# Performance work log

Hardware: AMD Instinct MI355X
Metric: run time of the kernel (lower is better)

## Reference

```python
import jax, jax.numpy as jnp
import numpy as np
import math

LOG2PI = math.log(2.0 * math.pi)
ALPHA, BETA, GAMMA = 1.0, 4.0, 1.0  # coefficients (mi, tc, dw_kl)


def gaussian_log_density(samples, mean, log_var):
    inv_sigma = jnp.exp(-log_var)
    tmp = samples - mean
    return -0.5 * (tmp * tmp * inv_sigma + log_var + LOG2PI)


def log_importance_weight_matrix(batch_size, dataset_size):
    # Faithful port of the TF/beta-tcvae MSS importance weights.
    N = float(dataset_size)
    M = batch_size - 1
    strat_weight = (N - M) / (N * M)
    W = jnp.full((batch_size, batch_size), 1.0 / M, dtype=jnp.float32)
    W = W.at[:, 0].set(1.0 / N)
    W = W.at[:, 1].set(strat_weight)
    W = W.at[M - 1, 0].set(strat_weight)
    return jnp.log(W)


def setup_inputs() -> dict:
    key = jax.random.key(0)
    k1, k2, k3, k4, k5 = jax.random.split(key, 5)
    B, D, F = 2048, 16, 512
    return {
        "x": jax.random.normal(k1, (B, F), dtype=jnp.float32),
        "reconstruction": jax.random.normal(k2, (B, F), dtype=jnp.float32),
        "mu": jax.random.normal(k3, (B, D), dtype=jnp.float32),
        "log_var": jax.random.normal(k4, (B, D), dtype=jnp.float32) * 0.5,
        "z": jax.random.normal(k5, (B, D), dtype=jnp.float32),
        "size_dataset": 100000,
    }


def reference(x, reconstruction, mu, log_var, z, size_dataset):
    B = z.shape[0]
    # reconstruction loss: mean over batch of per-sample MAE == global mean abs error
    recon_loss = jnp.mean(jnp.abs(x - reconstruction))

    # log q(z|x): [B]
    log_q_zx = jnp.sum(gaussian_log_density(z, mu, log_var), axis=-1)

    # pairwise densities: [B, B, D]  (z_i under q(.|x_j))
    log_qz_prob = gaussian_log_density(z[:, None, :], mu[None, :, :], log_var[None, :, :])

    # log p(z): note the original passes ones_like(z) as log_var (faithful quirk)
    log_prior = jnp.sum(
        gaussian_log_density(z, jnp.zeros_like(z), jnp.ones_like(z)), axis=-1
    )

    # MSS importance weights [B, B]
    logiw = log_importance_weight_matrix(B, size_dataset)

    # log q(z): logsumexp over batch of joint densities + weights
    log_qz = jax.nn.logsumexp(jnp.sum(log_qz_prob, axis=2) + logiw, axis=1)  # [B]

    # log prod_d q(z_d): dimension-wise logsumexp then sum over dims
    log_qz_product = jnp.sum(
        jax.nn.logsumexp(log_qz_prob + logiw[:, :, None], axis=1), axis=1
    )  # [B]

    mutual_info_loss = jnp.mean(log_q_zx - log_qz)
    tc_loss = jnp.mean(log_qz - log_qz_product)
    dimension_wise_kl = jnp.mean(log_qz_product - log_prior)

    total_loss = (
        recon_loss
        + ALPHA * mutual_info_loss
        + BETA * tc_loss
        + GAMMA * dimension_wise_kl
    )
    return total_loss
```

## Files before the change

kernel.cpp:

```cpp
#include <hip/hip_runtime.h>
#include <math.h>

#define LOG2PI_F 1.8378770664093453f
#define LOG2E_F  1.4426950408889634f
#define LN2_F    0.6931471805599453f
#define EXP_NEG1 0.36787944117144233f

#define TI   32
#define JSP  16
#define JCH  128
#define ROWF 52

__device__ __forceinline__ float exp2_(float x) { return __builtin_amdgcn_exp2f(x); }
__device__ __forceinline__ float log2_(float x) { return __builtin_amdgcn_logf(x); }


__global__ __launch_bounds__(256) void k_prep_recon(
        const float* __restrict__ mu, const float* __restrict__ lv,
        const float* __restrict__ z, const int* __restrict__ nds,
        const float4* __restrict__ x, const float4* __restrict__ r,
        float* __restrict__ AC, float* __restrict__ PPa, float* __restrict__ PPb,
        float* __restrict__ RP, int B, int n4, int prepBlks) {
    __shared__ float ra[4], rb[4];
    const int lane = threadIdx.x & 63, wv = threadIdx.x >> 6;

    if ((int)blockIdx.x < prepBlks) {
        int idx = blockIdx.x * 256 + threadIdx.x;
        int j = idx >> 4, d = idx & 15;
        float m = mu[idx], l = lv[idx], zz = z[idx];
        float is = __expf(-l);
        float a = -0.5f * LOG2E_F * is;
        float b = -2.0f * a * m;
        float ec = fmaf(-0.5f * LOG2E_F, l + LOG2PI_F, a * m * m);

        float Nf = (float)(*nds);
        float Mf = (float)(B - 1);
        float strat = (Nf - Mf) / (Nf * Mf);
        float w = (j == 0) ? (1.0f / Nf) : ((j == 1) ? strat : (1.0f / Mf));

        float* row = AC + (size_t)j * ROWF;
        row[d] = a;
        row[16 + d] = b;
        row[32 + d] = w * exp2_(ec);
        float es = ec;
        es += __shfl_xor(es, 1); es += __shfl_xor(es, 2);
        es += __shfl_xor(es, 4); es += __shfl_xor(es, 8);
        if (d == 0) row[48] = w * exp2_(es);

        float t = zz - m;
        float ga = -0.5f * (fmaf(t * t, is, l) + LOG2PI_F);
        float gb = -0.5f * (fmaf(zz * zz, EXP_NEG1, 1.0f) + LOG2PI_F);
        #pragma unroll
        for (int off = 32; off > 0; off >>= 1) { ga += __shfl_down(ga, off); gb += __shfl_down(gb, off); }
        if (lane == 0) { ra[wv] = ga; rb[wv] = gb; }
        __syncthreads();
        if (threadIdx.x == 0) {
            PPa[blockIdx.x] = ra[0] + ra[1] + ra[2] + ra[3];
            PPb[blockIdx.x] = rb[0] + rb[1] + rb[2] + rb[3];
        }
    } else {
        int bid = blockIdx.x - prepBlks;
        float s = 0.0f;
        for (int idx = bid * 256 + threadIdx.x; idx < n4; idx += 512 * 256) {
            float4 a = x[idx], b = r[idx];
            s += fabsf(a.x - b.x) + fabsf(a.y - b.y) + fabsf(a.z - b.z) + fabsf(a.w - b.w);
        }
        #pragma unroll
        for (int off = 32; off > 0; off >>= 1) s += __shfl_down(s, off);
        if (lane == 0) ra[wv] = s;
        __syncthreads();
        if (threadIdx.x == 0) RP[bid] = ra[0] + ra[1] + ra[2] + ra[3];
    }
}

#define DIM2(AQ, BQ, CQ, comp, dd, SA, SB) \
    e = fmaf(AQ.comp, va2[dd], BQ.comp * va[dd]); SA += e; sda[dd] = fmaf(CQ.comp, exp2_(e), sda[dd]); \
    e = fmaf(AQ.comp, vb2[dd], BQ.comp * vb[dd]); SB += e; sdb[dd] = fmaf(CQ.comp, exp2_(e), sdb[dd]);

__global__ __launch_bounds__(256) void k_pair(const float* __restrict__ AC,
                                              const float* __restrict__ z,
                                              float* __restrict__ Rs,
                                              int B, int jch) {
    __shared__ float sbuf[JCH * ROWF];
    __shared__ float red[4][TI][17];

    const int il = threadIdx.x & 15;
    const int jg = threadIdx.x >> 4;
    const int i0 = blockIdx.x * TI + il;
    const int jbase = blockIdx.y * jch;

    {
        const float4* g = (const float4*)(AC + (size_t)jbase * ROWF);
        float4* dst = (float4*)sbuf;
        #pragma unroll
        for (int k = 0; k < 7; ++k) {
            int idx = threadIdx.x + k * 256;
            if (idx < (JCH * ROWF) / 4) dst[idx] = g[idx];
        }
    }

    float va[16], va2[16], vb[16], vb2[16];
    {
        const float4* zp = (const float4*)(z + (size_t)i0 * 16);
        float4 z0 = zp[0], z1 = zp[1], z2 = zp[2], z3 = zp[3];
        va[0]=z0.x; va[1]=z0.y; va[2]=z0.z; va[3]=z0.w;
        va[4]=z1.x; va[5]=z1.y; va[6]=z1.z; va[7]=z1.w;
        va[8]=z2.x; va[9]=z2.y; va[10]=z2.z; va[11]=z2.w;
        va[12]=z3.x; va[13]=z3.y; va[14]=z3.z; va[15]=z3.w;
        const float4* zq = (const float4*)(z + (size_t)(i0 + 16) * 16);
        float4 y0 = zq[0], y1 = zq[1], y2 = zq[2], y3 = zq[3];
        vb[0]=y0.x; vb[1]=y0.y; vb[2]=y0.z; vb[3]=y0.w;
        vb[4]=y1.x; vb[5]=y1.y; vb[6]=y1.z; vb[7]=y1.w;
        vb[8]=y2.x; vb[9]=y2.y; vb[10]=y2.z; vb[11]=y2.w;
        vb[12]=y3.x; vb[13]=y3.y; vb[14]=y3.z; vb[15]=y3.w;
        #pragma unroll
        for (int d = 0; d < 16; d++) { va2[d] = va[d] * va[d]; vb2[d] = vb[d] * vb[d]; }
    }

    float sda[16], sdb[16];
    #pragma unroll
    for (int d = 0; d < 16; d++) { sda[d] = 0.0f; sdb[d] = 0.0f; }
    float stA = 0.0f, stB = 0.0f;

    __syncthreads();

    const int nk = jch >> 4;
    for (int k = 0; k < nk; ++k) {
        const float* rp = sbuf + (jg + 16 * k) * ROWF;
        const float4* r4 = (const float4*)rp;
        float sa0 = 0.0f, sa1 = 0.0f, sb0 = 0.0f, sb1 = 0.0f, e;
        {
            float4 A0 = r4[0], A1 = r4[1], Bq0 = r4[4], Bq1 = r4[5], C0 = r4[8], C1 = r4[9];
            DIM2(A0, Bq0, C0, x, 0, sa0, sb0)  DIM2(A0, Bq0, C0, y, 1, sa1, sb1)
            DIM2(A0, Bq0, C0, z, 2, sa0, sb0)  DIM2(A0, Bq0, C0, w, 3, sa1, sb1)
            DIM2(A1, Bq1, C1, x, 4, sa0, sb0)  DIM2(A1, Bq1, C1, y, 5, sa1, sb1)
            DIM2(A1, Bq1, C1, z, 6, sa0, sb0)  DIM2(A1, Bq1, C1, w, 7, sa1, sb1)
        }
        {
            float4 A2 = r4[2], A3 = r4[3], Bq2 = r4[6], Bq3 = r4[7], C2 = r4[10], C3 = r4[11];
            DIM2(A2, Bq2, C2, x, 8, sa0, sb0)  DIM2(A2, Bq2, C2, y, 9, sa1, sb1)
            DIM2(A2, Bq2, C2, z, 10, sa0, sb0) DIM2(A2, Bq2, C2, w, 11, sa1, sb1)
            DIM2(A3, Bq3, C3, x, 12, sa0, sb0) DIM2(A3, Bq3, C3, y, 13, sa1, sb1)
            DIM2(A3, Bq3, C3, z, 14, sa0, sb0) DIM2(A3, Bq3, C3, w, 15, sa1, sb1)
        }
        float P = rp[48];
        stA = fmaf(P, exp2_(sa0 + sa1), stA);
        stB = fmaf(P, exp2_(sb0 + sb1), stB);
    }

    #pragma unroll
    for (int msk = 16; msk <= 32; msk <<= 1) {
        stA += __shfl_xor(stA, msk);
        stB += __shfl_xor(stB, msk);
        #pragma unroll
        for (int d = 0; d < 16; d++) {
            sda[d] += __shfl_xor(sda[d], msk);
            sdb[d] += __shfl_xor(sdb[d], msk);
        }
    }
    const int lane = threadIdx.x & 63, wv = threadIdx.x >> 6;
    if (lane < 16) {
        red[wv][lane][0] = stA;
        red[wv][lane + 16][0] = stB;
        #pragma unroll
        for (int d = 0; d < 16; d++) {
            red[wv][lane][1 + d] = sda[d];
            red[wv][lane + 16][1 + d] = sdb[d];
        }
    }
    __syncthreads();
    for (int t = threadIdx.x; t < TI * 17; t += 256) {
        int il2 = t & 31, c = t >> 5;
        float s = red[0][il2][c] + red[1][il2][c] + red[2][il2][c] + red[3][il2][c];
        Rs[((size_t)blockIdx.y * 17 + c) * B + blockIdx.x * TI + il2] = s;
    }
}

__global__ __launch_bounds__(256) void k_logs(const float* __restrict__ Rs,
                                              const float* __restrict__ AC,
                                              const float* __restrict__ z,
                                              const int* __restrict__ nds,
                                              float* __restrict__ LPa,
                                              float* __restrict__ LPb, int B) {
    int i = blockIdx.x * 256 + threadIdx.x;
    float S = 0.0f, Sd[16];
    #pragma unroll
    for (int d = 0; d < 16; d++) Sd[d] = 0.0f;
    for (int sp = 0; sp < JSP; ++sp) {
        const float* base = Rs + (size_t)sp * 17 * B + i;
        S += base[0];
        #pragma unroll
        for (int d = 0; d < 16; d++) Sd[d] += base[(size_t)(1 + d) * B];
    }

    if (i == B - 2) {
        const float* row0 = AC;
        const float* vv = z + (size_t)i * 16;
        float Nf = (float)(*nds);
        float Mf = (float)(B - 1);
        float strat = (Nf - Mf) / (Nf * Mf);
        float dwN = (strat - 1.0f / Nf) * Nf;
        float s2 = 0.0f;
        #pragma unroll
        for (int d = 0; d < 16; d++) {
            float vd = vv[d];
            float e = fmaf(row0[d], vd * vd, row0[16 + d] * vd);
            s2 += e;
            Sd[d] += dwN * row0[32 + d] * exp2_(e);
        }
        S += dwN * row0[48] * exp2_(s2);
    }

    float lqz = log2_(S) * LN2_F;
    float lqzp = 0.0f;
    #pragma unroll
    for (int d = 0; d < 16; d++) lqzp += log2_(Sd[d]);
    lqzp *= LN2_F;

    #pragma unroll
    for (int off = 32; off > 0; off >>= 1) {
        lqz += __shfl_down(lqz, off);
        lqzp += __shfl_down(lqzp, off);
    }
    __shared__ float ra[4], rb[4];
    int lane = threadIdx.x & 63, wv = threadIdx.x >> 6;
    if (lane == 0) { ra[wv] = lqz; rb[wv] = lqzp; }
    __syncthreads();
    if (threadIdx.x == 0) {
        LPa[blockIdx.x] = ra[0] + ra[1] + ra[2] + ra[3];
        LPb[blockIdx.x] = rb[0] + rb[1] + rb[2] + rb[3];
    }
}

__global__ void k_final(const float* __restrict__ RP, const float* __restrict__ PPa,
                        const float* __restrict__ PPb, const float* __restrict__ LPa,
                        const float* __restrict__ LPb, float* __restrict__ out,
                        float invBF, float invB, int prepBlks, int logBlks) {
    int tid = threadIdx.x;
    float sr = 0.0f, sga = 0.0f, sgb = 0.0f, slz = 0.0f, slp = 0.0f;
    for (int t = tid; t < 512; t += 256) sr += RP[t];
    for (int t = tid; t < prepBlks; t += 256) { sga += PPa[t]; sgb += PPb[t]; }
    for (int t = tid; t < logBlks; t += 256) { slz += LPa[t]; slp += LPb[t]; }
    #pragma unroll
    for (int off = 32; off > 0; off >>= 1) {
        sr += __shfl_down(sr, off);   sga += __shfl_down(sga, off);
        sgb += __shfl_down(sgb, off); slz += __shfl_down(slz, off);
        slp += __shfl_down(slp, off);
    }
    __shared__ float red[4][5];
    int lane = tid & 63, wv = tid >> 6;
    if (lane == 0) {
        red[wv][0] = sr; red[wv][1] = sga; red[wv][2] = sgb;
        red[wv][3] = slz; red[wv][4] = slp;
    }
    __syncthreads();
    if (tid == 0) {
        float R  = red[0][0] + red[1][0] + red[2][0] + red[3][0];
        float GA = red[0][1] + red[1][1] + red[2][1] + red[3][1];
        float GB = red[0][2] + red[1][2] + red[2][2] + red[3][2];
        float LZ = red[0][3] + red[1][3] + red[2][3] + red[3][3];
        float LQ = red[0][4] + red[1][4] + red[2][4] + red[3][4];
        out[0] = R * invBF + (GA + 3.0f * LZ - 3.0f * LQ - GB) * invB;
    }
}

extern "C" void kernel_launch(void* const* d_in, const int* in_sizes, int n_in,
                              void* d_out, int out_size, void* d_ws, size_t ws_size,
                              hipStream_t stream) {
    const float* x   = (const float*)d_in[0];
    const float* rec = (const float*)d_in[1];
    const float* mu  = (const float*)d_in[2];
    const float* lv  = (const float*)d_in[3];
    const float* z   = (const float*)d_in[4];
    const int*   nds = (const int*)d_in[5];

    const int BD = in_sizes[2];
    const int B  = BD / 16;
    const int BF = in_sizes[0];
    const int n4 = BF / 4;
    const int prepBlks = BD / 256;
    const int logBlks  = B / 256;

    float* AC  = (float*)d_ws;
    float* Rs  = AC + (size_t)B * 52;
    float* PPa = Rs + (size_t)JSP * 17 * B;
    float* PPb = PPa + prepBlks;
    float* RP  = PPb + prepBlks;
    float* LPa = RP + 512;
    float* LPb = LPa + logBlks;

    k_prep_recon<<<prepBlks + 512, 256, 0, stream>>>(mu, lv, z, nds,
        (const float4*)x, (const float4*)rec, AC, PPa, PPb, RP, B, n4, prepBlks);
    dim3 gp(B / TI, JSP);
    k_pair <<<gp, 256, 0, stream>>>(AC, z, Rs, B, B / JSP);
    k_logs <<<logBlks, 256, 0, stream>>>(Rs, AC, z, nds, LPa, LPb, B);
    k_final<<<1, 256, 0, stream>>>(RP, PPa, PPb, LPa, LPb, (float*)d_out,
                                   1.0f / (float)BF, 1.0f / (float)B, prepBlks, logBlks);
}
```

Measured before the change: 93.80 us.

## Fuse prep and recon into pair kernel; fold final reduction into tail

Each pair block now recomputes its chunk's per-j coefficients directly into LDS instead of reading a precomputed table from global memory. The recon L1 reduction is spread across all pair blocks, and the final scalar reduction is done by the last tail block via an atomic counter. Four launches become two, removing launch gaps and the global round-trip of the coefficient table. In exchange every pair block redundantly recomputes exp for 128 rows and streams part of x/recon before its main loop.

New measurement: 94.50 us. Within noise of the previous version (+0.8%).

```diff
diff --git a/kernel.cpp b/kernel.cpp
--- a/kernel.cpp
+++ b/kernel.cpp
@@ -15,30 +15,44 @@
 __device__ __forceinline__ float log2_(float x) { return __builtin_amdgcn_logf(x); }
 
 
-__global__ __launch_bounds__(256) void k_prep_recon(
+#define DIM2(AQ, BQ, CQ, comp, dd, SA, SB) \
+    e = fmaf(AQ.comp, va2[dd], BQ.comp * va[dd]); SA += e; sda[dd] = fmaf(CQ.comp, exp2_(e), sda[dd]); \
+    e = fmaf(AQ.comp, vb2[dd], BQ.comp * vb[dd]); SB += e; sdb[dd] = fmaf(CQ.comp, exp2_(e), sdb[dd]);
+
+__global__ __launch_bounds__(256) void k_main(
         const float* __restrict__ mu, const float* __restrict__ lv,
         const float* __restrict__ z, const int* __restrict__ nds,
         const float4* __restrict__ x, const float4* __restrict__ r,
-        float* __restrict__ AC, float* __restrict__ PPa, float* __restrict__ PPb,
-        float* __restrict__ RP, int B, int n4, int prepBlks) {
-    __shared__ float ra[4], rb[4];
-    const int lane = threadIdx.x & 63, wv = threadIdx.x >> 6;
-
-    if ((int)blockIdx.x < prepBlks) {
-        int idx = blockIdx.x * 256 + threadIdx.x;
-        int j = idx >> 4, d = idx & 15;
-        float m = mu[idx], l = lv[idx], zz = z[idx];
+        float* __restrict__ Rs, float* __restrict__ PPa, float* __restrict__ PPb,
+        float* __restrict__ RP, unsigned* __restrict__ cnt,
+        int B, int n4) {
+    __shared__ float sbuf[JCH * ROWF];
+    __shared__ float red[4][TI][17];
+    __shared__ float pra[4], prb[4], prr[4];
+
+    const int tid  = threadIdx.x;
+    const int lane = tid & 63, wv = tid >> 6;
+    const int jbase = blockIdx.y * JCH;
+
+    if (blockIdx.x == 0 && blockIdx.y == 0 && tid == 0) *cnt = 0u;
+
+    float Nf = (float)(*nds);
+    float Mf = (float)(B - 1);
+    float strat = (Nf - Mf) / (Nf * Mf);
+    float ga = 0.0f, gb = 0.0f;
+    #pragma unroll
+    for (int it = 0; it < (JCH * 16) / 256; ++it) {
+        int item = it * 256 + tid;
+        int jl = item >> 4, d = item & 15;
+        int gi = jbase * 16 + item;
+        float m = mu[gi], l = lv[gi], zz = z[gi];
         float is = __expf(-l);
         float a = -0.5f * LOG2E_F * is;
         float b = -2.0f * a * m;
         float ec = fmaf(-0.5f * LOG2E_F, l + LOG2PI_F, a * m * m);
-
-        float Nf = (float)(*nds);
-        float Mf = (float)(B - 1);
-        float strat = (Nf - Mf) / (Nf * Mf);
+        int j = jbase + jl;
         float w = (j == 0) ? (1.0f / Nf) : ((j == 1) ? strat : (1.0f / Mf));
-
-        float* row = AC + (size_t)j * ROWF;
+        float* row = sbuf + jl * ROWF;
         row[d] = a;
         row[16 + d] = b;
         row[32 + d] = w * exp2_(ec);
@@ -46,59 +60,32 @@
         es += __shfl_xor(es, 1); es += __shfl_xor(es, 2);
         es += __shfl_xor(es, 4); es += __shfl_xor(es, 8);
         if (d == 0) row[48] = w * exp2_(es);
-
-        float t = zz - m;
-        float ga = -0.5f * (fmaf(t * t, is, l) + LOG2PI_F);
-        float gb = -0.5f * (fmaf(zz * zz, EXP_NEG1, 1.0f) + LOG2PI_F);
-        #pragma unroll
-        for (int off = 32; off > 0; off >>= 1) { ga += __shfl_down(ga, off); gb += __shfl_down(gb, off); }
-        if (lane == 0) { ra[wv] = ga; rb[wv] = gb; }
-        __syncthreads();
-        if (threadIdx.x == 0) {
-            PPa[blockIdx.x] = ra[0] + ra[1] + ra[2] + ra[3];
-            PPb[blockIdx.x] = rb[0] + rb[1] + rb[2] + rb[3];
-        }
-    } else {
-        int bid = blockIdx.x - prepBlks;
-        float s = 0.0f;
-        for (int idx = bid * 256 + threadIdx.x; idx < n4; idx += 512 * 256) {
-            float4 a = x[idx], b = r[idx];
-            s += fabsf(a.x - b.x) + fabsf(a.y - b.y) + fabsf(a.z - b.z) + fabsf(a.w - b.w);
-        }
-        #pragma unroll
-        for (int off = 32; off > 0; off >>= 1) s += __shfl_down(s, off);
-        if (lane == 0) ra[wv] = s;
-        __syncthreads();
-        if (threadIdx.x == 0) RP[bid] = ra[0] + ra[1] + ra[2] + ra[3];
-    }
-}
-
-#define DIM2(AQ, BQ, CQ, comp, dd, SA, SB) \
-    e = fmaf(AQ.comp, va2[dd], BQ.comp * va[dd]); SA += e; sda[dd] = fmaf(CQ.comp, exp2_(e), sda[dd]); \
-    e = fmaf(AQ.comp, vb2[dd], BQ.comp * vb[dd]); SB += e; sdb[dd] = fmaf(CQ.comp, exp2_(e), sdb[dd]);
-
-__global__ __launch_bounds__(256) void k_pair(const float* __restrict__ AC,
-                                              const float* __restrict__ z,
-                                              float* __restrict__ Rs,
-                                              int B, int jch) {
-    __shared__ float sbuf[JCH * ROWF];
-    __shared__ float red[4][TI][17];
-
-    const int il = threadIdx.x & 15;
-    const int jg = threadIdx.x >> 4;
+        if (blockIdx.x == 0) {
+            float t = zz - m;
+            ga += -0.5f * (fmaf(t * t, is, l) + LOG2PI_F);
+            gb += -0.5f * (fmaf(zz * zz, EXP_NEG1, 1.0f) + LOG2PI_F);
+        }
+    }
+
+    float sr = 0.0f;
+    const int nblk = gridDim.x * gridDim.y;
+    const int bid  = blockIdx.y * gridDim.x + blockIdx.x;
+    for (int idx = bid * 256 + tid; idx < n4; idx += nblk * 256) {
+        float4 a4 = x[idx], b4 = r[idx];
+        sr += fabsf(a4.x - b4.x) + fabsf(a4.y - b4.y) +
+              fabsf(a4.z - b4.z) + fabsf(a4.w - b4.w);
+    }
+    #pragma unroll
+    for (int off = 32; off > 0; off >>= 1) {
+        sr += __shfl_down(sr, off);
+        ga += __shfl_down(ga, off);
+        gb += __shfl_down(gb, off);
+    }
+    if (lane == 0) { prr[wv] = sr; pra[wv] = ga; prb[wv] = gb; }
+
+    const int il = tid & 15;
+    const int jg = tid >> 4;
     const int i0 = blockIdx.x * TI + il;
-    const int jbase = blockIdx.y * jch;
-
-    {
-        const float4* g = (const float4*)(AC + (size_t)jbase * ROWF);
-        float4* dst = (float4*)sbuf;
-        #pragma unroll
-        for (int k = 0; k < 7; ++k) {
-            int idx = threadIdx.x + k * 256;
-            if (idx < (JCH * ROWF) / 4) dst[idx] = g[idx];
-        }
-    }
-
     float va[16], va2[16], vb[16], vb2[16];
     {
         const float4* zp = (const float4*)(z + (size_t)i0 * 16);
@@ -124,7 +111,15 @@
 
     __syncthreads();
 
-    const int nk = jch >> 4;
+    if (tid == 0) {
+        RP[bid] = prr[0] + prr[1] + prr[2] + prr[3];
+        if (blockIdx.x == 0) {
+            PPa[blockIdx.y] = pra[0] + pra[1] + pra[2] + pra[3];
+            PPb[blockIdx.y] = prb[0] + prb[1] + prb[2] + prb[3];
+        }
+    }
+
+    const int nk = JCH >> 4;
     for (int k = 0; k < nk; ++k) {
         const float* rp = sbuf + (jg + 16 * k) * ROWF;
         const float4* r4 = (const float4*)rp;
@@ -158,7 +153,6 @@
             sdb[d] += __shfl_xor(sdb[d], msk);
         }
     }
-    const int lane = threadIdx.x & 63, wv = threadIdx.x >> 6;
     if (lane < 16) {
         red[wv][lane][0] = stA;
         red[wv][lane + 16][0] = stB;
@@ -169,20 +163,23 @@
         }
     }
     __syncthreads();
-    for (int t = threadIdx.x; t < TI * 17; t += 256) {
+    for (int t = tid; t < TI * 17; t += 256) {
         int il2 = t & 31, c = t >> 5;
         float s = red[0][il2][c] + red[1][il2][c] + red[2][il2][c] + red[3][il2][c];
         Rs[((size_t)blockIdx.y * 17 + c) * B + blockIdx.x * TI + il2] = s;
     }
 }
 
-__global__ __launch_bounds__(256) void k_logs(const float* __restrict__ Rs,
-                                              const float* __restrict__ AC,
-                                              const float* __restrict__ z,
-                                              const int* __restrict__ nds,
-                                              float* __restrict__ LPa,
-                                              float* __restrict__ LPb, int B) {
-    int i = blockIdx.x * 256 + threadIdx.x;
+__global__ __launch_bounds__(256) void k_tail(
+        const float* __restrict__ Rs, const float* __restrict__ mu,
+        const float* __restrict__ lv, const float* __restrict__ z,
+        const int* __restrict__ nds,
+        const float* __restrict__ RP, const float* __restrict__ PPa,
+        const float* __restrict__ PPb, float* __restrict__ LPa,
+        float* __restrict__ LPb, unsigned* __restrict__ cnt,
+        float* __restrict__ out, int B, int nRP, float invBF, float invB) {
+    const int tid = threadIdx.x;
+    const int i = blockIdx.x * 256 + tid;
     float S = 0.0f, Sd[16];
     #pragma unroll
     for (int d = 0; d < 16; d++) Sd[d] = 0.0f;
@@ -193,22 +190,26 @@
         for (int d = 0; d < 16; d++) Sd[d] += base[(size_t)(1 + d) * B];
     }
 
+    float Nf = (float)(*nds);
+    float Mf = (float)(B - 1);
+    float strat = (Nf - Mf) / (Nf * Mf);
     if (i == B - 2) {
-        const float* row0 = AC;
+        float dw = strat - 1.0f / Nf;
         const float* vv = z + (size_t)i * 16;
-        float Nf = (float)(*nds);
-        float Mf = (float)(B - 1);
-        float strat = (Nf - Mf) / (Nf * Mf);
-        float dwN = (strat - 1.0f / Nf) * Nf;
         float s2 = 0.0f;
         #pragma unroll
         for (int d = 0; d < 16; d++) {
+            float m = mu[d], l = lv[d];
+            float is = __expf(-l);
+            float a = -0.5f * LOG2E_F * is;
+            float b = -2.0f * a * m;
+            float ec = fmaf(-0.5f * LOG2E_F, l + LOG2PI_F, a * m * m);
             float vd = vv[d];
-            float e = fmaf(row0[d], vd * vd, row0[16 + d] * vd);
-            s2 += e;
-            Sd[d] += dwN * row0[32 + d] * exp2_(e);
-        }
-        S += dwN * row0[48] * exp2_(s2);
+            float ee = fmaf(a, vd * vd, b * vd) + ec;
+            s2 += ee;
+            Sd[d] += dw * exp2_(ee);
+        }
+        S += dw * exp2_(s2);
     }
 
     float lqz = log2_(S) * LN2_F;
@@ -223,44 +224,44 @@
         lqzp += __shfl_down(lqzp, off);
     }
     __shared__ float ra[4], rb[4];
-    int lane = threadIdx.x & 63, wv = threadIdx.x >> 6;
+    const int lane = tid & 63, wv = tid >> 6;
     if (lane == 0) { ra[wv] = lqz; rb[wv] = lqzp; }
     __syncthreads();
-    if (threadIdx.x == 0) {
+    if (tid == 0) {
         LPa[blockIdx.x] = ra[0] + ra[1] + ra[2] + ra[3];
         LPb[blockIdx.x] = rb[0] + rb[1] + rb[2] + rb[3];
     }
-}
-
-__global__ void k_final(const float* __restrict__ RP, const float* __restrict__ PPa,
-                        const float* __restrict__ PPb, const float* __restrict__ LPa,
-                        const float* __restrict__ LPb, float* __restrict__ out,
-                        float invBF, float invB, int prepBlks, int logBlks) {
-    int tid = threadIdx.x;
-    float sr = 0.0f, sga = 0.0f, sgb = 0.0f, slz = 0.0f, slp = 0.0f;
-    for (int t = tid; t < 512; t += 256) sr += RP[t];
-    for (int t = tid; t < prepBlks; t += 256) { sga += PPa[t]; sgb += PPb[t]; }
-    for (int t = tid; t < logBlks; t += 256) { slz += LPa[t]; slp += LPb[t]; }
-    #pragma unroll
-    for (int off = 32; off > 0; off >>= 1) {
-        sr += __shfl_down(sr, off);   sga += __shfl_down(sga, off);
-        sgb += __shfl_down(sgb, off); slz += __shfl_down(slz, off);
-        slp += __shfl_down(slp, off);
-    }
-    __shared__ float red[4][5];
-    int lane = tid & 63, wv = tid >> 6;
-    if (lane == 0) {
-        red[wv][0] = sr; red[wv][1] = sga; red[wv][2] = sgb;
-        red[wv][3] = slz; red[wv][4] = slp;
-    }
-    __syncthreads();
-    if (tid == 0) {
-        float R  = red[0][0] + red[1][0] + red[2][0] + red[3][0];
-        float GA = red[0][1] + red[1][1] + red[2][1] + red[3][1];
-        float GB = red[0][2] + red[1][2] + red[2][2] + red[3][2];
-        float LZ = red[0][3] + red[1][3] + red[2][3] + red[3][3];
-        float LQ = red[0][4] + red[1][4] + red[2][4] + red[3][4];
-        out[0] = R * invBF + (GA + 3.0f * LZ - 3.0f * LQ - GB) * invB;
+
+    __threadfence();
+    __shared__ unsigned lastf;
+    if (tid == 0) lastf = (atomicAdd(cnt, 1u) == (unsigned)gridDim.x - 1u) ? 1u : 0u;
+    __syncthreads();
+    if (lastf) {
+        __threadfence();
+        float s0 = 0.0f, s1 = 0.0f, s2 = 0.0f, s3 = 0.0f, s4 = 0.0f;
+        for (int t = tid; t < nRP; t += 256) s0 += RP[t];
+        for (int t = tid; t < JSP; t += 256) { s1 += PPa[t]; s2 += PPb[t]; }
+        for (int t = tid; t < (int)gridDim.x; t += 256) { s3 += LPa[t]; s4 += LPb[t]; }
+        #pragma unroll
+        for (int off = 32; off > 0; off >>= 1) {
+            s0 += __shfl_down(s0, off); s1 += __shfl_down(s1, off);
+            s2 += __shfl_down(s2, off); s3 += __shfl_down(s3, off);
+            s4 += __shfl_down(s4, off);
+        }
+        __shared__ float fr[4][5];
+        if (lane == 0) {
+            fr[wv][0] = s0; fr[wv][1] = s1; fr[wv][2] = s2;
+            fr[wv][3] = s3; fr[wv][4] = s4;
+        }
+        __syncthreads();
+        if (tid == 0) {
+            float R  = fr[0][0] + fr[1][0] + fr[2][0] + fr[3][0];
+            float GA = fr[0][1] + fr[1][1] + fr[2][1] + fr[3][1];
+            float GB = fr[0][2] + fr[1][2] + fr[2][2] + fr[3][2];
+            float LZ = fr[0][3] + fr[1][3] + fr[2][3] + fr[3][3];
+            float LQ = fr[0][4] + fr[1][4] + fr[2][4] + fr[3][4];
+            out[0] = R * invBF + (GA + 3.0f * LZ - 3.0f * LQ - GB) * invB;
+        }
     }
 }
 
@@ -278,22 +279,21 @@
     const int B  = BD / 16;
     const int BF = in_sizes[0];
     const int n4 = BF / 4;
-    const int prepBlks = BD / 256;
-    const int logBlks  = B / 256;
-
-    float* AC  = (float*)d_ws;
-    float* Rs  = AC + (size_t)B * 52;
+    const int nRP = (B / TI) * JSP;
+    const int logBlks = B / 256;
+
+    float* Rs  = (float*)d_ws;
     float* PPa = Rs + (size_t)JSP * 17 * B;
-    float* PPb = PPa + prepBlks;
-    float* RP  = PPb + prepBlks;
-    float* LPa = RP + 512;
+    float* PPb = PPa + JSP;
+    float* RP  = PPb + JSP;
+    float* LPa = RP + nRP;
     float* LPb = LPa + logBlks;
-
-    k_prep_recon<<<prepBlks + 512, 256, 0, stream>>>(mu, lv, z, nds,
-        (const float4*)x, (const float4*)rec, AC, PPa, PPb, RP, B, n4, prepBlks);
-    dim3 gp(B / TI, JSP);
-    k_pair <<<gp, 256, 0, stream>>>(AC, z, Rs, B, B / JSP);
-    k_logs <<<logBlks, 256, 0, stream>>>(Rs, AC, z, nds, LPa, LPb, B);
-    k_final<<<1, 256, 0, stream>>>(RP, PPa, PPb, LPa, LPb, (float*)d_out,
-                                   1.0f / (float)BF, 1.0f / (float)B, prepBlks, logBlks);
+    unsigned* cnt = (unsigned*)(LPb + logBlks);
+
+    dim3 gm(B / TI, JSP);
+    k_main<<<gm, 256, 0, stream>>>(mu, lv, z, nds,
+        (const float4*)x, (const float4*)rec, Rs, PPa, PPb, RP, cnt, B, n4);
+    k_tail<<<logBlks, 256, 0, stream>>>(Rs, mu, lv, z, nds, RP, PPa, PPb,
+        LPa, LPb, cnt, (float*)d_out, B, nRP,
+        1.0f / (float)BF, 1.0f / (float)B);
 }
```
